# Optimization experiments

Hardware: AMD Instinct MI355X
Metric: run time of the kernel (lower is better)

Reference implementation:

```python
import jax, jax.numpy as jnp
import numpy as np

B, S, T = 4, 1024, 1024
CTX, QIN, C, H = 1024, 1024, 1024, 16
HD = C // H  # per-head channels


def setup_inputs() -> dict:
    key = jax.random.key(0)
    ks = jax.random.split(key, 12)
    s = 0.02
    return {
        "query": jax.random.normal(ks[0], (B, S, QIN), jnp.float32),
        "key": jax.random.normal(ks[1], (B, T, CTX), jnp.float32),
        "value": jax.random.normal(ks[2], (B, T, CTX), jnp.float32),
        "mask": jax.random.randint(ks[3], (B, S, T), 0, 2).astype(bool),
        "Wq": jax.random.normal(ks[4], (C, QIN), jnp.float32) * s,
        "bq": jax.random.normal(ks[5], (C,), jnp.float32) * s,
        "Wk": jax.random.normal(ks[6], (C, CTX), jnp.float32) * s,
        "bk": jax.random.normal(ks[7], (C,), jnp.float32) * s,
        "Wv": jax.random.normal(ks[8], (C, CTX), jnp.float32) * s,
        "bv": jax.random.normal(ks[9], (C,), jnp.float32) * s,
        "Wo": jax.random.normal(ks[10], (C, C), jnp.float32) * s,
        "bo": jax.random.normal(ks[11], (C,), jnp.float32) * s,
    }


def reference(query, key, value, mask, Wq, bq, Wk, bk, Wv, bv, Wo, bo):
    b, s, _ = query.shape
    t = key.shape[1]
    c = Wq.shape[0]
    h, hd = H, c // H
    q = (query @ Wq.T + bq).reshape(b, s, h, hd)
    k = (key @ Wk.T + bk).reshape(b, t, h, hd)
    v = (value @ Wv.T + bv).reshape(b, t, h, hd)
    # [B,H,S,T] scores, scaled by 1/sqrt(head_dim)
    score = jnp.einsum('bshd,bthd->bhst', q, k) * (hd ** -0.5)
    # masked_fill_(~mask[:, None, 0:1], -inf): mask key positions via row 0
    score = jnp.where(mask[:, None, 0:1], score, -jnp.inf)
    weights = jax.nn.softmax(score, axis=-1)
    out = jnp.einsum('bhst,bthd->bshd', weights, v).reshape(b, s, c)
    out = out @ Wo.T + bo
    out = out * mask[..., 0:1].astype(out.dtype)
    return out
```

## Files before the change

kernel.cpp:

```cpp
#include <hip/hip_runtime.h>
#include <stdint.h>

#define Bb  4
#define Ss  1024
#define Tt  1024
#define Cc  1024
#define Hh  16
#define HDd 64
#define Kk  1024

typedef __bf16 bf16;
typedef __bf16 bf16x8 __attribute__((ext_vector_type(8)));
typedef float  f32x4  __attribute__((ext_vector_type(4)));
typedef __attribute__((address_space(1))) uint32_t gu32;
typedef __attribute__((address_space(3))) uint32_t lu32;

__device__ __forceinline__ void load_lds16(const bf16* g, bf16* l) {
    __builtin_amdgcn_global_load_lds((gu32*)g, (lu32*)l, 16, 0, 0);
}

__global__ void cvt8(const float* __restrict__ s0, const float* __restrict__ s1,
                     const float* __restrict__ s2, const float* __restrict__ s3,
                     const float* __restrict__ s4, const float* __restrict__ s5,
                     const float* __restrict__ s6,
                     bf16* __restrict__ d0, bf16* __restrict__ d1,
                     bf16* __restrict__ d2, bf16* __restrict__ d3,
                     bf16* __restrict__ d4, bf16* __restrict__ d5,
                     bf16* __restrict__ d6)
{
    const float* s; bf16* d; int n;
    switch (blockIdx.y) {
        case 0: s = s0; d = d0; n = Bb * Ss * Kk; break;
        case 1: s = s1; d = d1; n = Bb * Ss * Kk; break;
        case 2: s = s2; d = d2; n = Bb * Ss * Kk; break;
        case 3: s = s3; d = d3; n = Cc * Kk; break;
        case 4: s = s4; d = d4; n = Cc * Kk; break;
        case 5: s = s5; d = d5; n = Cc * Kk; break;
        default: s = s6; d = d6; n = Cc * Kk; break;
    }
    const int i = (blockIdx.x * blockDim.x + threadIdx.x) * 8;
    if (i >= n) return;
    const float4 a = *(const float4*)(s + i);
    const float4 c = *(const float4*)(s + i + 4);
    bf16x8 o;
    o[0] = (bf16)a.x; o[1] = (bf16)a.y; o[2] = (bf16)a.z; o[3] = (bf16)a.w;
    o[4] = (bf16)c.x; o[5] = (bf16)c.y; o[6] = (bf16)c.z; o[7] = (bf16)c.w;
    *(bf16x8*)(d + i) = o;
}

__device__ __forceinline__ void mainloop_128x64(
    const bf16* __restrict__ Ab, const bf16* __restrict__ Wb,
    bf16* As, bf16* Bs, f32x4 acc[4][2])
{
    const int tid  = threadIdx.x;
    const int wid  = tid >> 6;
    const int lane = tid & 63;
    const int l16  = lane & 15;
    const int quad = lane >> 4;
    const int wm   = wid >> 1;
    const int wn   = wid & 1;
    const int r8   = lane >> 3;
    const int ssw  = ((lane & 7) ^ r8) * 8;

    for (int k0 = 0; k0 < Kk; k0 += 64) {
#pragma unroll
        for (int p = 0; p < 4; p++) {
            const int rb = wid * 32 + p * 8;
            load_lds16(Ab + (size_t)(rb + r8) * Kk + k0 + ssw, As + rb * 64);
        }
#pragma unroll
        for (int p = 0; p < 2; p++) {
            const int rb = wid * 16 + p * 8;
            load_lds16(Wb + (size_t)(rb + r8) * Kk + k0 + ssw, Bs + rb * 64);
        }
        __syncthreads();
#pragma unroll
        for (int kh = 0; kh < 2; kh++) {
            bf16x8 af[4], bw[2];
#pragma unroll
            for (int i = 0; i < 4; i++)
                af[i] = *(const bf16x8*)(As + (wm * 64 + i * 16 + l16) * 64 +
                                         (((kh * 4 + quad) ^ (l16 & 7)) * 8));
#pragma unroll
            for (int j = 0; j < 2; j++)
                bw[j] = *(const bf16x8*)(Bs + (wn * 32 + j * 16 + l16) * 64 +
                                         (((kh * 4 + quad) ^ (l16 & 7)) * 8));
#pragma unroll
            for (int i = 0; i < 4; i++)
#pragma unroll
                for (int j = 0; j < 2; j++)
                    acc[i][j] = __builtin_amdgcn_mfma_f32_16x16x32_bf16(af[i], bw[j], acc[i][j], 0, 0, 0);
        }
        __syncthreads();
    }
}

__device__ __forceinline__ void mainloop_64x64(
    const bf16* __restrict__ Ab, const bf16* __restrict__ Wb,
    bf16* As, bf16* Bs, f32x4 acc[2][2])
{
    const int tid  = threadIdx.x;
    const int wid  = tid >> 6;
    const int lane = tid & 63;
    const int l16  = lane & 15;
    const int quad = lane >> 4;
    const int wm   = wid >> 1;
    const int wn   = wid & 1;
    const int r8   = lane >> 3;
    const int ssw  = ((lane & 7) ^ r8) * 8;

    for (int k0 = 0; k0 < Kk; k0 += 64) {
#pragma unroll
        for (int p = 0; p < 2; p++) {
            const int rb = wid * 16 + p * 8;
            load_lds16(Ab + (size_t)(rb + r8) * Kk + k0 + ssw, As + rb * 64);
        }
#pragma unroll
        for (int p = 0; p < 2; p++) {
            const int rb = wid * 16 + p * 8;
            load_lds16(Wb + (size_t)(rb + r8) * Kk + k0 + ssw, Bs + rb * 64);
        }
        __syncthreads();
#pragma unroll
        for (int kh = 0; kh < 2; kh++) {
            bf16x8 af[2], bw[2];
#pragma unroll
            for (int i = 0; i < 2; i++)
                af[i] = *(const bf16x8*)(As + (wm * 32 + i * 16 + l16) * 64 +
                                         (((kh * 4 + quad) ^ (l16 & 7)) * 8));
#pragma unroll
            for (int j = 0; j < 2; j++)
                bw[j] = *(const bf16x8*)(Bs + (wn * 32 + j * 16 + l16) * 64 +
                                         (((kh * 4 + quad) ^ (l16 & 7)) * 8));
#pragma unroll
            for (int i = 0; i < 2; i++)
#pragma unroll
                for (int j = 0; j < 2; j++)
                    acc[i][j] = __builtin_amdgcn_mfma_f32_16x16x32_bf16(af[i], bw[j], acc[i][j], 0, 0, 0);
        }
        __syncthreads();
    }
}

__global__ __launch_bounds__(256)
void gemm_qkv(const bf16* __restrict__ Aq, const bf16* __restrict__ Ak, const bf16* __restrict__ Av,
              const bf16* __restrict__ Wq, const bf16* __restrict__ Wk, const bf16* __restrict__ Wv,
              const float* __restrict__ bq, const float* __restrict__ bk, const float* __restrict__ bv,
              bf16* __restrict__ Oq, bf16* __restrict__ Ok, bf16* __restrict__ Ov)
{
    __shared__ __align__(16) bf16 As[128 * 64];
    __shared__ __align__(16) bf16 Bs[64 * 64];
    const int z = blockIdx.z;
    const bf16*  A    = (z == 0) ? Aq : (z == 1) ? Ak : Av;
    const bf16*  W    = (z == 0) ? Wq : (z == 1) ? Wk : Wv;
    const float* bias = (z == 0) ? bq : (z == 1) ? bk : bv;
    bf16*        O    = (z == 0) ? Oq : (z == 1) ? Ok : Ov;

    f32x4 acc[4][2];
    const f32x4 z4 = {0.f, 0.f, 0.f, 0.f};
#pragma unroll
    for (int i = 0; i < 4; i++)
#pragma unroll
        for (int j = 0; j < 2; j++) acc[i][j] = z4;

    mainloop_128x64(A + (size_t)blockIdx.x * 128 * Kk,
                    W + (size_t)blockIdx.y * 64 * Kk, As, Bs, acc);

    const int tid = threadIdx.x;
    const int wid = tid >> 6, lane = tid & 63;
    const int l16 = lane & 15, quad = lane >> 4;
    const int wm = wid >> 1, wn = wid & 1;
    const int row0 = blockIdx.x * 128 + wm * 64;
    const int col0 = blockIdx.y * 64 + wn * 32;
#pragma unroll
    for (int j = 0; j < 2; j++) {
        const int col = col0 + j * 16 + l16;
        const float bj = bias[col];
        const int h = col >> 6, d = col & 63;
#pragma unroll
        for (int i = 0; i < 4; i++) {
#pragma unroll
            for (int r = 0; r < 4; r++) {
                const int row = row0 + i * 16 + quad * 4 + r;
                const int b = row >> 10, s = row & 1023;
                const bf16 val = (bf16)(acc[i][j][r] + bj);
                if (z == 2) {
                    Ov[((size_t)((b * Hh + h) * HDd + d)) * Tt + s] = val;
                } else {
                    O[((size_t)(b * Hh + h) * Ss + s) * HDd + d] = val;
                }
            }
        }
    }
}

__global__ __launch_bounds__(256)
void gemm_out(const bf16* __restrict__ A, const bf16* __restrict__ W,
              const float* __restrict__ bias, const int* __restrict__ mask,
              float* __restrict__ out)
{
    __shared__ __align__(16) bf16 As[64 * 64];
    __shared__ __align__(16) bf16 Bs[64 * 64];
    f32x4 acc[2][2];
    const f32x4 z4 = {0.f, 0.f, 0.f, 0.f};
#pragma unroll
    for (int i = 0; i < 2; i++)
#pragma unroll
        for (int j = 0; j < 2; j++) acc[i][j] = z4;

    mainloop_64x64(A + (size_t)blockIdx.x * 64 * Kk,
                   W + (size_t)blockIdx.y * 64 * Kk, As, Bs, acc);

    const int tid = threadIdx.x;
    const int wid = tid >> 6, lane = tid & 63;
    const int l16 = lane & 15, quad = lane >> 4;
    const int wm = wid >> 1, wn = wid & 1;
    const int row0 = blockIdx.x * 64 + wm * 32;
    const int col0 = blockIdx.y * 64 + wn * 32;
#pragma unroll
    for (int j = 0; j < 2; j++) {
        const int col = col0 + j * 16 + l16;
        const float bj = bias[col];
#pragma unroll
        for (int i = 0; i < 2; i++) {
#pragma unroll
            for (int r = 0; r < 4; r++) {
                const int row = row0 + i * 16 + quad * 4 + r;
                const float mval = (mask[(size_t)row * Tt] != 0) ? 1.f : 0.f;
                out[(size_t)row * Cc + col] = (acc[i][j][r] + bj) * mval;
            }
        }
    }
}

__global__ __launch_bounds__(256)
void attn(const bf16* __restrict__ Q, const bf16* __restrict__ Kp, const bf16* __restrict__ Vt,
          const int* __restrict__ mask, bf16* __restrict__ X)
{
    __shared__ __align__(16) bf16 Ks[64 * 64];
    __shared__ __align__(16) bf16 Vs[64 * 64];
    __shared__ __align__(16) bf16 Ps[4][16 * 72];
    const int g   = blockIdx.x;
    const int xcd = g & 7, idx = g >> 3;
    const int bh  = xcd * 8 + (idx >> 4);
    const int qblk = idx & 15;
    const int b = bh >> 4, h = bh & 15;
    const int tid = threadIdx.x, wid = tid >> 6, lane = tid & 63;
    const int l16 = lane & 15, quad = lane >> 4;
    const bf16* Qbh = Q  + (size_t)bh * Ss * HDd;
    const bf16* Kbh = Kp + (size_t)bh * Tt * HDd;
    const bf16* Vbh = Vt + (size_t)bh * HDd * Tt;
    const int*  mb  = mask + (size_t)b * Ss * Tt;
    const int q0 = qblk * 64 + wid * 16;
    bf16* Psw = &Ps[wid][0];

    const bf16x8 qf0 = *(const bf16x8*)(Qbh + (size_t)(q0 + l16) * HDd + quad * 8);
    const bf16x8 qf1 = *(const bf16x8*)(Qbh + (size_t)(q0 + l16) * HDd + 32 + quad * 8);

    float ls[4];
    f32x4 o[4];
    const f32x4 z4 = {0.f, 0.f, 0.f, 0.f};
#pragma unroll
    for (int r = 0; r < 4; r++) ls[r] = 0.f;
#pragma unroll
    for (int dblk = 0; dblk < 4; dblk++) o[dblk] = z4;

    const int srow = lane >> 3;
    const int schk = lane & 7;
    const int sswz = (schk ^ srow) * 8;

    for (int kt = 0; kt < Tt; kt += 64) {
#pragma unroll
        for (int p = 0; p < 2; p++) {
            const int c8 = wid * 2 + p;
            load_lds16(Kbh + (size_t)(kt + c8 * 8 + srow) * HDd + sswz,
                       Ks + c8 * 512);
            load_lds16(Vbh + (size_t)(c8 * 8 + srow) * Tt + kt + sswz,
                       Vs + c8 * 512);
        }
        __syncthreads();

        f32x4 sc[4];
#pragma unroll
        for (int nb = 0; nb < 4; nb++) sc[nb] = z4;
#pragma unroll
        for (int nb = 0; nb < 4; nb++) {
            const bf16* krow = Ks + (nb * 16 + l16) * 64;
            const bf16x8 kf0 = *(const bf16x8*)(krow + ((quad     ^ (l16 & 7)) * 8));
            const bf16x8 kf1 = *(const bf16x8*)(krow + (((4 + quad) ^ (l16 & 7)) * 8));
            sc[nb] = __builtin_amdgcn_mfma_f32_16x16x32_bf16(qf0, kf0, sc[nb], 0, 0, 0);
            sc[nb] = __builtin_amdgcn_mfma_f32_16x16x32_bf16(qf1, kf1, sc[nb], 0, 0, 0);
        }

#pragma unroll
        for (int nb = 0; nb < 4; nb++) {
            const float madd = mb[kt + nb * 16 + l16] ? 0.f : -1e30f;
#pragma unroll
            for (int r = 0; r < 4; r++) {
                const float p = __expf(sc[nb][r] * 0.125f + madd);
                ls[r] += p;
                Psw[(quad * 4 + r) * 72 + nb * 16 + l16] = (bf16)p;
            }
        }

#pragma unroll
        for (int kh = 0; kh < 2; kh++) {
            const bf16x8 pf = *(const bf16x8*)(Psw + l16 * 72 + kh * 32 + quad * 8);
#pragma unroll
            for (int dblk = 0; dblk < 4; dblk++) {
                const bf16x8 vf = *(const bf16x8*)(Vs + (dblk * 16 + l16) * 64 +
                                                   (((kh * 4 + quad) ^ (l16 & 7)) * 8));
                o[dblk] = __builtin_amdgcn_mfma_f32_16x16x32_bf16(pf, vf, o[dblk], 0, 0, 0);
            }
        }
        __syncthreads();
    }

#pragma unroll
    for (int off = 1; off <= 8; off <<= 1)
#pragma unroll
        for (int r = 0; r < 4; r++)
            ls[r] += __shfl_xor(ls[r], off, 64);
    float inv[4];
#pragma unroll
    for (int r = 0; r < 4; r++) inv[r] = 1.f / ls[r];

#pragma unroll
    for (int dblk = 0; dblk < 4; dblk++) {
#pragma unroll
        for (int r = 0; r < 4; r++) {
            const int srow_q = q0 + quad * 4 + r;
            const int d = dblk * 16 + l16;
            X[(size_t)(b * Ss + srow_q) * Cc + h * HDd + d] = (bf16)(o[dblk][r] * inv[r]);
        }
    }
}

extern "C" void kernel_launch(void* const* d_in, const int* in_sizes, int n_in,
                              void* d_out, int out_size, void* d_ws, size_t ws_size,
                              hipStream_t stream)
{
    const float* query = (const float*)d_in[0];
    const float* key   = (const float*)d_in[1];
    const float* value = (const float*)d_in[2];
    const int*   mask  = (const int*)d_in[3];
    const float* Wq = (const float*)d_in[4];
    const float* bq = (const float*)d_in[5];
    const float* Wk = (const float*)d_in[6];
    const float* bk = (const float*)d_in[7];
    const float* Wv = (const float*)d_in[8];
    const float* bv = (const float*)d_in[9];
    const float* Wo = (const float*)d_in[10];
    const float* bo = (const float*)d_in[11];
    float* out = (float*)d_out;

    char* ws = (char*)d_ws;
    const size_t MB = 1024 * 1024;
    bf16* qb  = (bf16*)(ws + 0 * MB);
    bf16* kb  = (bf16*)(ws + 8 * MB);
    bf16* vb  = (bf16*)(ws + 16 * MB);
    bf16* wqb = (bf16*)(ws + 24 * MB);
    bf16* wkb = (bf16*)(ws + 26 * MB);
    bf16* wvb = (bf16*)(ws + 28 * MB);
    bf16* wob = (bf16*)(ws + 30 * MB);
    bf16* Qp  = (bf16*)(ws + 32 * MB);
    bf16* Kpp = (bf16*)(ws + 40 * MB);
    bf16* Vtp = (bf16*)(ws + 48 * MB);
    bf16* Xb  = (bf16*)(ws + 56 * MB);

    cvt8<<<dim3(2048, 7), 256, 0, stream>>>(query, key, value, Wq, Wk, Wv, Wo,
                                            qb, kb, vb, wqb, wkb, wvb, wob);
    gemm_qkv<<<dim3(32, 16, 3), 256, 0, stream>>>(qb, kb, vb, wqb, wkb, wvb,
                                                  bq, bk, bv, Qp, Kpp, Vtp);
    attn<<<dim3(1024), 256, 0, stream>>>(Qp, Kpp, Vtp, mask, Xb);
    gemm_out<<<dim3(64, 16), 256, 0, stream>>>(Xb, wob, bo, mask, out);
}
```

Measured before the change: 232.9 us.

## Compact valid keys and queries via mask prefix-sum and skip masked work

A prefix-sum pass over mask row 0 and column 0 builds ranks and valid counts per batch. The QKV GEMM epilogue scatters only valid query and key rows into compacted positions. Attention then loops only over valid keys and skips query blocks past the valid count, and the output GEMM processes only valid query rows, scattering them back through an inverse index. Masked output rows and the padding of V are pre-zeroed inside the conversion kernel. The attention loop also switches from direct global-to-LDS loads to register-staged double buffering with explicit barriers. Together this cuts attention and output-projection work roughly in proportion to mask density. In exchange it adds scan work, scattered stores and extra zeroing traffic.

```diff
diff --git a/kernel.cpp b/kernel.cpp
--- a/kernel.cpp
+++ b/kernel.cpp
@@ -19,15 +19,69 @@
     __builtin_amdgcn_global_load_lds((gu32*)g, (lu32*)l, 16, 0, 0);
 }
 
+#define BARRIER_LDS() do {                                    \
+    asm volatile("s_waitcnt lgkmcnt(0)" ::: "memory");        \
+    __builtin_amdgcn_s_barrier();                             \
+} while (0)
+
+
 __global__ void cvt8(const float* __restrict__ s0, const float* __restrict__ s1,
                      const float* __restrict__ s2, const float* __restrict__ s3,
                      const float* __restrict__ s4, const float* __restrict__ s5,
                      const float* __restrict__ s6,
+                     const int* __restrict__ mask,
+                     int* __restrict__ rankK, int* __restrict__ nkK,
+                     int* __restrict__ rankQ, int* __restrict__ nkQ,
+                     int* __restrict__ invQ,
+                     bf16* __restrict__ vz, float* __restrict__ oz,
                      bf16* __restrict__ d0, bf16* __restrict__ d1,
                      bf16* __restrict__ d2, bf16* __restrict__ d3,
                      bf16* __restrict__ d4, bf16* __restrict__ d5,
                      bf16* __restrict__ d6)
 {
+    const int tid = threadIdx.x;
+    if (blockIdx.y == 7) {
+        const int x = blockIdx.x;
+        if (x < 8) {
+            const int b = x >> 1, kind = x & 1;
+            const int* mb = mask + (size_t)b * Ss * Tt;
+            __shared__ int part[256];
+            int v[4]; int s = 0;
+#pragma unroll
+            for (int u = 0; u < 4; u++) {
+                const int idx = tid * 4 + u;
+                v[u] = kind ? (mb[(size_t)idx * Tt] != 0) : (mb[idx] != 0);
+                s += v[u];
+            }
+            part[tid] = s; __syncthreads();
+            for (int off = 1; off < 256; off <<= 1) {
+                const int t_ = (tid >= off) ? part[tid - off] : 0;
+                __syncthreads();
+                part[tid] += t_;
+                __syncthreads();
+            }
+            int a = part[tid] - s;
+#pragma unroll
+            for (int u = 0; u < 4; u++) {
+                const int idx = tid * 4 + u;
+                const int j = v[u] ? a : -1;
+                if (kind) { rankQ[b * Tt + idx] = j; if (j >= 0) invQ[b * Tt + j] = idx; }
+                else      { rankK[b * Tt + idx] = j; }
+                a += v[u];
+            }
+            if (tid == 255) { if (kind) nkQ[b] = a; else nkK[b] = a; }
+        } else if (x < 2056) {
+            const float4 z = {0.f, 0.f, 0.f, 0.f};
+            float* p = (float*)((char*)vz + (size_t)(x - 8) * 4096) + tid * 4;
+            *(float4*)p = z;
+        } else {
+            const float4 z = {0.f, 0.f, 0.f, 0.f};
+            float* p = (float*)((char*)oz + (size_t)(x - 2056) * 8192) + tid * 8;
+            *(float4*)p = z; *(float4*)(p + 4) = z;
+        }
+        return;
+    }
+
     const float* s; bf16* d; int n;
     switch (blockIdx.y) {
         case 0: s = s0; d = d0; n = Bb * Ss * Kk; break;
@@ -38,7 +92,7 @@
         case 5: s = s5; d = d5; n = Cc * Kk; break;
         default: s = s6; d = d6; n = Cc * Kk; break;
     }
-    const int i = (blockIdx.x * blockDim.x + threadIdx.x) * 8;
+    const int i = (blockIdx.x * blockDim.x + tid) * 8;
     if (i >= n) return;
     const float4 a = *(const float4*)(s + i);
     const float4 c = *(const float4*)(s + i + 4);
@@ -48,7 +102,7 @@
     *(bf16x8*)(d + i) = o;
 }
 
-__device__ __forceinline__ void mainloop_128x64(
+__device__ __forceinline__ void mainloop_128x64_nv(
     const bf16* __restrict__ Ab, const bf16* __restrict__ Wb,
     bf16* As, bf16* Bs, f32x4 acc[4][2])
 {
@@ -95,7 +149,7 @@
     }
 }
 
-__device__ __forceinline__ void mainloop_64x64(
+__device__ __forceinline__ void mainloop_64x64_nv(
     const bf16* __restrict__ Ab, const bf16* __restrict__ Wb,
     bf16* As, bf16* Bs, f32x4 acc[2][2])
 {
@@ -114,10 +168,6 @@
         for (int p = 0; p < 2; p++) {
             const int rb = wid * 16 + p * 8;
             load_lds16(Ab + (size_t)(rb + r8) * Kk + k0 + ssw, As + rb * 64);
-        }
-#pragma unroll
-        for (int p = 0; p < 2; p++) {
-            const int rb = wid * 16 + p * 8;
             load_lds16(Wb + (size_t)(rb + r8) * Kk + k0 + ssw, Bs + rb * 64);
         }
         __syncthreads();
@@ -146,6 +196,7 @@
 void gemm_qkv(const bf16* __restrict__ Aq, const bf16* __restrict__ Ak, const bf16* __restrict__ Av,
               const bf16* __restrict__ Wq, const bf16* __restrict__ Wk, const bf16* __restrict__ Wv,
               const float* __restrict__ bq, const float* __restrict__ bk, const float* __restrict__ bv,
+              const int* __restrict__ rankK, const int* __restrict__ rankQ,
               bf16* __restrict__ Oq, bf16* __restrict__ Ok, bf16* __restrict__ Ov)
 {
     __shared__ __align__(16) bf16 As[128 * 64];
@@ -154,7 +205,7 @@
     const bf16*  A    = (z == 0) ? Aq : (z == 1) ? Ak : Av;
     const bf16*  W    = (z == 0) ? Wq : (z == 1) ? Wk : Wv;
     const float* bias = (z == 0) ? bq : (z == 1) ? bk : bv;
-    bf16*        O    = (z == 0) ? Oq : (z == 1) ? Ok : Ov;
+    const int*   rnk  = (z == 0) ? rankQ : rankK;
 
     f32x4 acc[4][2];
     const f32x4 z4 = {0.f, 0.f, 0.f, 0.f};
@@ -163,32 +214,37 @@
 #pragma unroll
         for (int j = 0; j < 2; j++) acc[i][j] = z4;
 
-    mainloop_128x64(A + (size_t)blockIdx.x * 128 * Kk,
-                    W + (size_t)blockIdx.y * 64 * Kk, As, Bs, acc);
+    mainloop_128x64_nv(A + (size_t)blockIdx.x * 128 * Kk,
+                       W + (size_t)blockIdx.y * 64 * Kk, As, Bs, acc);
 
     const int tid = threadIdx.x;
     const int wid = tid >> 6, lane = tid & 63;
     const int l16 = lane & 15, quad = lane >> 4;
     const int wm = wid >> 1, wn = wid & 1;
-    const int row0 = blockIdx.x * 128 + wm * 64;
     const int col0 = blockIdx.y * 64 + wn * 32;
+
+    float bjv[2]; int hv[2], dv[2];
 #pragma unroll
     for (int j = 0; j < 2; j++) {
         const int col = col0 + j * 16 + l16;
-        const float bj = bias[col];
-        const int h = col >> 6, d = col & 63;
-#pragma unroll
-        for (int i = 0; i < 4; i++) {
-#pragma unroll
-            for (int r = 0; r < 4; r++) {
-                const int row = row0 + i * 16 + quad * 4 + r;
-                const int b = row >> 10, s = row & 1023;
-                const bf16 val = (bf16)(acc[i][j][r] + bj);
-                if (z == 2) {
-                    Ov[((size_t)((b * Hh + h) * HDd + d)) * Tt + s] = val;
-                } else {
-                    O[((size_t)(b * Hh + h) * Ss + s) * HDd + d] = val;
-                }
+        bjv[j] = bias[col];
+        hv[j] = col >> 6; dv[j] = col & 63;
+    }
+#pragma unroll
+    for (int i = 0; i < 4; i++) {
+#pragma unroll
+        for (int r = 0; r < 4; r++) {
+            const int row = blockIdx.x * 128 + wm * 64 + i * 16 + quad * 4 + r;
+            const int bb = row >> 10, t = row & 1023;
+            const int jc = rnk[bb * Tt + t];
+            if (jc < 0) continue;
+#pragma unroll
+            for (int j = 0; j < 2; j++) {
+                const bf16 val = (bf16)(acc[i][j][r] + bjv[j]);
+                const int h = hv[j], d = dv[j];
+                if (z == 0)      Oq[((size_t)(bb * Hh + h) * Ss + jc) * HDd + d] = val;
+                else if (z == 1) Ok[((size_t)(bb * Hh + h) * Tt + jc) * HDd + d] = val;
+                else             Ov[((size_t)((bb * Hh + h) * HDd + d)) * Tt + jc] = val;
             }
         }
     }
@@ -196,9 +252,16 @@
 
 __global__ __launch_bounds__(256)
 void gemm_out(const bf16* __restrict__ A, const bf16* __restrict__ W,
-              const float* __restrict__ bias, const int* __restrict__ mask,
+              const float* __restrict__ bias,
+              const int* __restrict__ nkQ, const int* __restrict__ invQ,
               float* __restrict__ out)
 {
+    const int bb    = blockIdx.x & 3;
+    const int strip = blockIdx.x >> 2;
+    const int t0 = strip * 64;
+    const int nq = nkQ[bb];
+    if (t0 >= nq) return;
+
     __shared__ __align__(16) bf16 As[64 * 64];
     __shared__ __align__(16) bf16 Bs[64 * 64];
     f32x4 acc[2][2];
@@ -208,14 +271,13 @@
 #pragma unroll
         for (int j = 0; j < 2; j++) acc[i][j] = z4;
 
-    mainloop_64x64(A + (size_t)blockIdx.x * 64 * Kk,
-                   W + (size_t)blockIdx.y * 64 * Kk, As, Bs, acc);
+    mainloop_64x64_nv(A + (size_t)(bb * 1024 + t0) * Kk,
+                      W + (size_t)blockIdx.y * 64 * Kk, As, Bs, acc);
 
     const int tid = threadIdx.x;
     const int wid = tid >> 6, lane = tid & 63;
     const int l16 = lane & 15, quad = lane >> 4;
     const int wm = wid >> 1, wn = wid & 1;
-    const int row0 = blockIdx.x * 64 + wm * 32;
     const int col0 = blockIdx.y * 64 + wn * 32;
 #pragma unroll
     for (int j = 0; j < 2; j++) {
@@ -225,17 +287,19 @@
         for (int i = 0; i < 2; i++) {
 #pragma unroll
             for (int r = 0; r < 4; r++) {
-                const int row = row0 + i * 16 + quad * 4 + r;
-                const float mval = (mask[(size_t)row * Tt] != 0) ? 1.f : 0.f;
-                out[(size_t)row * Cc + col] = (acc[i][j][r] + bj) * mval;
-            }
-        }
-    }
-}
-
-__global__ __launch_bounds__(256)
+                const int jrow = t0 + wm * 32 + i * 16 + quad * 4 + r;
+                if (jrow < nq) {
+                    const int s = invQ[bb * Tt + jrow];
+                    out[((size_t)bb * Ss + s) * Cc + col] = acc[i][j][r] + bj;
+                }
+            }
+        }
+    }
+}
+
+__global__ __launch_bounds__(256, 2)
 void attn(const bf16* __restrict__ Q, const bf16* __restrict__ Kp, const bf16* __restrict__ Vt,
-          const int* __restrict__ mask, bf16* __restrict__ X)
+          const int* __restrict__ nkK, const int* __restrict__ nkQ, bf16* __restrict__ X)
 {
     __shared__ __align__(16) bf16 Ks[64 * 64];
     __shared__ __align__(16) bf16 Vs[64 * 64];
@@ -245,12 +309,16 @@
     const int bh  = xcd * 8 + (idx >> 4);
     const int qblk = idx & 15;
     const int b = bh >> 4, h = bh & 15;
+    const int nq  = nkQ[b];
+    if (qblk * 64 >= nq) return;
+    const int nkb = nkK[b];
+    const int lim = ((nkb + 127) >> 7) << 7;
+
     const int tid = threadIdx.x, wid = tid >> 6, lane = tid & 63;
     const int l16 = lane & 15, quad = lane >> 4;
     const bf16* Qbh = Q  + (size_t)bh * Ss * HDd;
     const bf16* Kbh = Kp + (size_t)bh * Tt * HDd;
     const bf16* Vbh = Vt + (size_t)bh * HDd * Tt;
-    const int*  mb  = mask + (size_t)b * Ss * Tt;
     const int q0 = qblk * 64 + wid * 16;
     bf16* Psw = &Ps[wid][0];
 
@@ -268,25 +336,45 @@
     const int srow = lane >> 3;
     const int schk = lane & 7;
     const int sswz = (schk ^ srow) * 8;
-
-    for (int kt = 0; kt < Tt; kt += 64) {
-#pragma unroll
-        for (int p = 0; p < 2; p++) {
-            const int c8 = wid * 2 + p;
-            load_lds16(Kbh + (size_t)(kt + c8 * 8 + srow) * HDd + sswz,
-                       Ks + c8 * 512);
-            load_lds16(Vbh + (size_t)(c8 * 8 + srow) * Tt + kt + sswz,
-                       Vs + c8 * 512);
-        }
-        __syncthreads();
-
+    const int c80 = wid * 2, c81 = wid * 2 + 1;
+
+    const bf16* kg0 = Kbh + (size_t)(c80 * 8 + srow) * HDd + sswz;
+    const bf16* kg1 = Kbh + (size_t)(c81 * 8 + srow) * HDd + sswz;
+    const bf16* vg0 = Vbh + (size_t)(c80 * 8 + srow) * Tt + sswz;
+    const bf16* vg1 = Vbh + (size_t)(c81 * 8 + srow) * Tt + sswz;
+    bf16* kd0 = Ks + c80 * 512 + lane * 8;
+    bf16* kd1 = Ks + c81 * 512 + lane * 8;
+    bf16* vd0 = Vs + c80 * 512 + lane * 8;
+    bf16* vd1 = Vs + c81 * 512 + lane * 8;
+
+    bf16x8 ka0, ka1, va0, va1;
+    bf16x8 kb0, kb1, vb0, vb1;
+
+#define LOADA(KT) do { const int _kt = (KT);                          \
+    ka0 = *(const bf16x8*)(kg0 + (size_t)_kt * HDd);                  \
+    ka1 = *(const bf16x8*)(kg1 + (size_t)_kt * HDd);                  \
+    va0 = *(const bf16x8*)(vg0 + _kt);                                \
+    va1 = *(const bf16x8*)(vg1 + _kt); } while (0)
+#define LOADB(KT) do { const int _kt = (KT);                          \
+    kb0 = *(const bf16x8*)(kg0 + (size_t)_kt * HDd);                  \
+    kb1 = *(const bf16x8*)(kg1 + (size_t)_kt * HDd);                  \
+    vb0 = *(const bf16x8*)(vg0 + _kt);                                \
+    vb1 = *(const bf16x8*)(vg1 + _kt); } while (0)
+#define STOREA() do {                                                 \
+    *(bf16x8*)kd0 = ka0; *(bf16x8*)kd1 = ka1;                         \
+    *(bf16x8*)vd0 = va0; *(bf16x8*)vd1 = va1; } while (0)
+#define STOREB() do {                                                 \
+    *(bf16x8*)kd0 = kb0; *(bf16x8*)kd1 = kb1;                         \
+    *(bf16x8*)vd0 = vb0; *(bf16x8*)vd1 = vb1; } while (0)
+
+    auto compute = [&](int base) {
         f32x4 sc[4];
 #pragma unroll
         for (int nb = 0; nb < 4; nb++) sc[nb] = z4;
 #pragma unroll
         for (int nb = 0; nb < 4; nb++) {
             const bf16* krow = Ks + (nb * 16 + l16) * 64;
-            const bf16x8 kf0 = *(const bf16x8*)(krow + ((quad     ^ (l16 & 7)) * 8));
+            const bf16x8 kf0 = *(const bf16x8*)(krow + ((quad       ^ (l16 & 7)) * 8));
             const bf16x8 kf1 = *(const bf16x8*)(krow + (((4 + quad) ^ (l16 & 7)) * 8));
             sc[nb] = __builtin_amdgcn_mfma_f32_16x16x32_bf16(qf0, kf0, sc[nb], 0, 0, 0);
             sc[nb] = __builtin_amdgcn_mfma_f32_16x16x32_bf16(qf1, kf1, sc[nb], 0, 0, 0);
@@ -294,10 +382,10 @@
 
 #pragma unroll
         for (int nb = 0; nb < 4; nb++) {
-            const float madd = mb[kt + nb * 16 + l16] ? 0.f : -1e30f;
+            const bool vv = (base + nb * 16 + l16) < nkb;
 #pragma unroll
             for (int r = 0; r < 4; r++) {
-                const float p = __expf(sc[nb][r] * 0.125f + madd);
+                const float p = vv ? __expf(sc[nb][r] * 0.125f) : 0.f;
                 ls[r] += p;
                 Psw[(quad * 4 + r) * 72 + nb * 16 + l16] = (bf16)p;
             }
@@ -313,8 +401,27 @@
                 o[dblk] = __builtin_amdgcn_mfma_f32_16x16x32_bf16(pf, vf, o[dblk], 0, 0, 0);
             }
         }
-        __syncthreads();
-    }
+    };
+
+    LOADA(0);
+
+    for (int kt = 0; kt < lim; kt += 128) {
+        BARRIER_LDS();
+        LOADB(kt + 64);
+        STOREA();
+        BARRIER_LDS();
+        compute(kt);
+
+        BARRIER_LDS();
+        LOADA((kt + 128 < lim) ? (kt + 128) : (lim - 64));
+        STOREB();
+        BARRIER_LDS();
+        compute(kt + 64);
+    }
+#undef LOADA
+#undef LOADB
+#undef STOREA
+#undef STOREB
 
 #pragma unroll
     for (int off = 1; off <= 8; off <<= 1)
@@ -330,8 +437,10 @@
 #pragma unroll
         for (int r = 0; r < 4; r++) {
             const int srow_q = q0 + quad * 4 + r;
-            const int d = dblk * 16 + l16;
-            X[(size_t)(b * Ss + srow_q) * Cc + h * HDd + d] = (bf16)(o[dblk][r] * inv[r]);
+            if (srow_q < nq) {
+                const int d = dblk * 16 + l16;
+                X[(size_t)(b * Ss + srow_q) * Cc + h * HDd + d] = (bf16)(o[dblk][r] * inv[r]);
+            }
         }
     }
 }
@@ -368,10 +477,20 @@
     bf16* Vtp = (bf16*)(ws + 48 * MB);
     bf16* Xb  = (bf16*)(ws + 56 * MB);
 
-    cvt8<<<dim3(2048, 7), 256, 0, stream>>>(query, key, value, Wq, Wk, Wv, Wo,
+    char* intb = ws + 64 * MB - 64 * 1024;
+    int* rankK = (int*)(intb);
+    int* rankQ = (int*)(intb + 16 * 1024);
+    int* invQ  = (int*)(intb + 32 * 1024);
+    int* nkK   = (int*)(intb + 48 * 1024);
+    int* nkQ   = (int*)(intb + 48 * 1024 + 256);
+
+    cvt8<<<dim3(4104, 8), 256, 0, stream>>>(query, key, value, Wq, Wk, Wv, Wo,
+                                            mask, rankK, nkK, rankQ, nkQ, invQ,
+                                            Vtp, out,
                                             qb, kb, vb, wqb, wkb, wvb, wob);
     gemm_qkv<<<dim3(32, 16, 3), 256, 0, stream>>>(qb, kb, vb, wqb, wkb, wvb,
-                                                  bq, bk, bv, Qp, Kpp, Vtp);
-    attn<<<dim3(1024), 256, 0, stream>>>(Qp, Kpp, Vtp, mask, Xb);
-    gemm_out<<<dim3(64, 16), 256, 0, stream>>>(Xb, wob, bo, mask, out);
-}
+                                                  bq, bk, bv, rankK, rankQ,
+                                                  Qp, Kpp, Vtp);
+    attn<<<dim3(1024), 256, 0, stream>>>(Qp, Kpp, Vtp, nkK, nkQ, Xb);
+    gemm_out<<<dim3(64, 16), 256, 0, stream>>>(Xb, wob, bo, nkQ, invQ, out);
+}
```

Result: faster. 218.9 us (-6.0%).
